# Kernel tuning notes

Measured on AMD Instinct MI355X. Metric: run time of the kernel, lower is better.

The kernel has to match this reference:

```python
import jax, jax.numpy as jnp
import numpy as np

N = 50000      # nodes
E = 400000     # edges (before self loops)
IN = 128       # in_channels
H = 4          # num_heads (layers 1-2)
C = 32         # hidden_dim per head
HID = H * C    # 128 total hidden
CLS = 40       # num_classes (out_heads = 1)
EPS = 1e-5     # BatchNorm eps
SLOPE = 0.2    # LeakyReLU negative slope (PyG GATConv default)


def setup_inputs() -> dict:
    key = jax.random.key(0)
    ks = jax.random.split(key, 24)
    rn = lambda k, shp, s: jax.random.normal(k, shp, jnp.float32) * s
    x = jax.random.normal(ks[0], (N, IN), jnp.float32)
    src = jax.random.randint(ks[1], (E,), 0, N)
    dst = jax.random.randint(ks[2], (E,), 0, N)
    src = jnp.where(src == dst, (src + 1) % N, src)  # no pre-existing self loops
    edge_index = jnp.stack([src, dst]).astype(jnp.int32)
    inp = dict(x=x, edge_index=edge_index)
    # conv1: in IN -> H heads x C
    inp['W1'] = rn(ks[3], (IN, H * C), 1.0 / np.sqrt(IN))
    inp['as1'] = rn(ks[4], (H, C), 0.1)
    inp['ad1'] = rn(ks[5], (H, C), 0.1)
    inp['b1'] = rn(ks[6], (H * C,), 0.02)
    # conv2: HID -> H x C
    inp['W2'] = rn(ks[7], (HID, H * C), 1.0 / np.sqrt(HID))
    inp['as2'] = rn(ks[8], (H, C), 0.1)
    inp['ad2'] = rn(ks[9], (H, C), 0.1)
    inp['b2'] = rn(ks[10], (H * C,), 0.02)
    # conv3: HID -> 1 head x CLS, concat=False
    inp['W3'] = rn(ks[11], (HID, CLS), 1.0 / np.sqrt(HID))
    inp['as3'] = rn(ks[12], (1, CLS), 0.1)
    inp['ad3'] = rn(ks[13], (1, CLS), 0.1)
    inp['b3'] = rn(ks[14], (CLS,), 0.02)
    # residual projection
    inp['Wres'] = rn(ks[15], (IN, HID), 1.0 / np.sqrt(IN))
    # BatchNorm (eval mode: running stats)
    inp['g1'] = 1.0 + rn(ks[16], (HID,), 0.1)
    inp['be1'] = rn(ks[17], (HID,), 0.1)
    inp['m1'] = rn(ks[18], (HID,), 0.1)
    inp['v1'] = 1.0 + jax.random.uniform(ks[19], (HID,), jnp.float32) * 0.5
    inp['g2'] = 1.0 + rn(ks[20], (HID,), 0.1)
    inp['be2'] = rn(ks[21], (HID,), 0.1)
    inp['m2'] = rn(ks[22], (HID,), 0.1)
    inp['v2'] = 1.0 + jax.random.uniform(ks[23], (HID,), jnp.float32) * 0.5
    return inp


def _gat_conv(h, src, dst, W, a_src, a_dst, bias, heads, out_ch, concat):
    """PyG-style GATConv (eval: attention dropout off), self loops already in src/dst."""
    n = h.shape[0]
    xw = (h @ W).reshape(n, heads, out_ch)                    # [N,H,C]
    e_src = jnp.sum(xw * a_src, axis=-1)                      # [N,H]
    e_dst = jnp.sum(xw * a_dst, axis=-1)                      # [N,H]
    e = jax.nn.leaky_relu(e_src[src] + e_dst[dst], SLOPE)     # [E',H]
    # segment softmax over incoming edges of each dst node
    mseg = jax.ops.segment_max(e, dst, num_segments=n)        # [N,H]
    ex = jnp.exp(e - mseg[dst])
    den = jax.ops.segment_sum(ex, dst, num_segments=n)
    alpha = ex / den[dst]                                     # [E',H]
    out = jax.ops.segment_sum(alpha[:, :, None] * xw[src], dst, num_segments=n)  # [N,H,C]
    out = out.reshape(n, heads * out_ch) if concat else out.mean(axis=1)
    return out + bias


def _bn(h, g, b, m, v):
    return (h - m) * jax.lax.rsqrt(v + EPS) * g + b


def reference(x, edge_index, W1, as1, ad1, b1, W2, as2, ad2, b2,
              W3, as3, ad3, b3, Wres, g1, be1, m1, v1, g2, be2, m2, v2):
    n = x.shape[0]
    loop = jnp.arange(n, dtype=edge_index.dtype)
    src = jnp.concatenate([edge_index[0], loop])  # add self loops (PyG default)
    dst = jnp.concatenate([edge_index[1], loop])
    x0 = x
    h = _gat_conv(x0, src, dst, W1, as1, ad1, b1, H, C, True)
    h = jax.nn.elu(_bn(h, g1, be1, m1, v1) + x0 @ Wres)
    h_res = h
    h = _gat_conv(h, src, dst, W2, as2, ad2, b2, H, C, True)
    h = jax.nn.elu(_bn(h, g2, be2, m2, v2) + h_res)
    logits = _gat_conv(h, src, dst, W3, as3, ad3, b3, 1, CLS, False)
    return logits
```

## Files before the change

### kernel.cpp

```cpp
#include <hip/hip_runtime.h>
#include <hip/hip_bf16.h>

#define THREADS 256

typedef __attribute__((ext_vector_type(8))) short bfrag;
typedef __attribute__((ext_vector_type(4))) float f32x4;

__device__ inline unsigned short f2b(float v) {
    __hip_bfloat16 b = __float2bfloat16(v);
    return *reinterpret_cast<unsigned short*>(&b);
}
__device__ inline float b2f(unsigned short u) {
    return __uint_as_float(((unsigned)u) << 16);
}
__device__ inline float rdv(const void* p, int off, bool isbf) {
    return isbf ? b2f(((const unsigned short*)p)[off]) : ((const float*)p)[off];
}
__device__ inline float dot8(const void* W, const void* av, int wbase, int abase, bool isbf) {
    if (isbf) {
        const unsigned short* wp = (const unsigned short*)W + wbase;
        const unsigned short* ap = (const unsigned short*)av + abase;
        ushort4 w0 = *(const ushort4*)wp, w1 = *(const ushort4*)(wp + 4);
        ushort4 a0 = *(const ushort4*)ap, a1 = *(const ushort4*)(ap + 4);
        return b2f(w0.x) * b2f(a0.x) + b2f(w0.y) * b2f(a0.y) +
               b2f(w0.z) * b2f(a0.z) + b2f(w0.w) * b2f(a0.w) +
               b2f(w1.x) * b2f(a1.x) + b2f(w1.y) * b2f(a1.y) +
               b2f(w1.z) * b2f(a1.z) + b2f(w1.w) * b2f(a1.w);
    } else {
        const float* wp = (const float*)W + wbase;
        const float* ap = (const float*)av + abase;
        float4 w0 = *(const float4*)wp, w1 = *(const float4*)(wp + 4);
        float4 a0 = *(const float4*)ap, a1 = *(const float4*)(ap + 4);
        return w0.x * a0.x + w0.y * a0.y + w0.z * a0.z + w0.w * a0.w +
               w1.x * a1.x + w1.y * a1.y + w1.z * a1.z + w1.w * a1.w;
    }
}

struct InPtrs { const void* p[23]; };

__global__ void prep_kernel(InPtrs in, int* __restrict__ flag,
                            unsigned short* __restrict__ Wl1, unsigned short* __restrict__ Wl2,
                            unsigned short* __restrict__ WlR, unsigned short* __restrict__ Wl3,
                            float* __restrict__ bnsc1, float* __restrict__ bnsh1,
                            float* __restrict__ bnsc2, float* __restrict__ bnsh2,
                            float* __restrict__ B3f,
                            int N, const int* __restrict__ ei, int* __restrict__ deg8,
                            int E, int DB) {
    int b = blockIdx.x, tid = threadIdx.x;
    if (b >= 30) {
        int stride = DB * 256;
        for (int i = (b - 30) * 256 + tid; i < E + N; i += stride) {
            int d = (i < E) ? ei[E + i] : (i - E);
            int k = (i >> 10) & 7;
            atomicAdd(&deg8[k * N + d], 1);
        }
        return;
    }
    __shared__ int sred[4];
    __shared__ float sWes[128 * 8];
    const unsigned short* x = (const unsigned short*)in.p[0];
    int local = 0;
    for (int i = tid; i < 4096; i += 256) {
        unsigned ex = (x[i] >> 7) & 0xFF;
        if (ex == 0xFF || ex >= 134 || (ex > 0 && ex <= 100)) local++;
    }
#pragma unroll
    for (int o = 1; o < 64; o <<= 1) local += __shfl_xor(local, o, 64);
    if ((tid & 63) == 0) sred[tid >> 6] = local;
    __syncthreads();
    bool isbf = !((sred[0] + sred[1] + sred[2] + sred[3]) * 8 > 4096);

    if (b < 29) {
        const void *Wv, *asp = 0, *adp = 0; unsigned short* o; int cols, FH = 0, tt;
        if (b < 9)       { Wv = in.p[2];  asp = in.p[3];  adp = in.p[4];  o = Wl1; cols = 128; FH = 4; tt = b; }
        else if (b < 18) { Wv = in.p[6];  asp = in.p[7];  adp = in.p[8];  o = Wl2; cols = 128; FH = 4; tt = b - 9; }
        else if (b < 26) { Wv = in.p[14];                                 o = WlR; cols = 128;         tt = b - 18; }
        else             { Wv = in.p[10]; asp = in.p[11]; adp = in.p[12]; o = Wl3; cols = 40;  FH = 1; tt = b - 26; }
        bool foldblk = (FH == 4 && tt == 8) || (FH == 1 && tt == 2);
        if (foldblk) {
            if (FH == 4) {
#pragma unroll
                for (int u = 0; u < 4; ++u) {
                    int od = tid * 4 + u;
                    int k = od >> 3, dn = od & 7;
                    int h = dn < 4 ? dn : dn - 4;
                    const void* av = dn < 4 ? asp : adp;
                    float s = 0.f;
#pragma unroll
                    for (int cc = 0; cc < 32; cc += 8)
                        s += dot8(Wv, av, k * 128 + h * 32 + cc, h * 32 + cc, isbf);
                    sWes[k * 8 + dn] = s;
                }
            } else {
                int k = tid >> 1, dn = tid & 1;
                const void* av = dn ? adp : asp;
                float s = 0.f;
#pragma unroll
                for (int cc = 0; cc < 40; cc += 8)
                    s += dot8(Wv, av, k * 40 + cc, cc, isbf);
                sWes[k * 8 + dn] = s;
            }
            __syncthreads();
        }
        int id = tt * 256 + tid;
        int ks = (id >> 6) & 3, l = id & 63;
        int q = l >> 4, n = l & 15;
        int c = tt * 16 + n;
#pragma unroll
        for (int j = 0; j < 8; ++j) {
            int k = ks * 32 + q * 8 + j;
            float v = 0.f;
            if (c < cols) v = rdv(Wv, k * cols + c, isbf);
            else if (FH && c < cols + 2 * FH) v = sWes[k * 8 + (c - cols)];
            o[id * 8 + j] = f2b(v);
        }
    } else {
        int c = tid;
        if (c < 128) {
            float s = rdv(in.p[15], c, isbf) * rsqrtf(rdv(in.p[18], c, isbf) + 1e-5f);
            bnsc1[c] = s;
            bnsh1[c] = rdv(in.p[16], c, isbf) - rdv(in.p[17], c, isbf) * s +
                       rdv(in.p[5], c, isbf) * s;
        } else {
            int d = c - 128;
            float s = rdv(in.p[19], d, isbf) * rsqrtf(rdv(in.p[22], d, isbf) + 1e-5f);
            bnsc2[d] = s;
            bnsh2[d] = rdv(in.p[20], d, isbf) - rdv(in.p[21], d, isbf) * s +
                       rdv(in.p[9], d, isbf) * s;
            if (d < 40) B3f[d] = rdv(in.p[13], d, isbf);
        }
        if (tid == 0) *flag = isbf ? 1 : 0;
    }
}

__global__ void bsum_kernel(const int* __restrict__ deg8, int* __restrict__ bsum, int N) {
    int idx = blockIdx.x * 256 + threadIdx.x;
    int lane = threadIdx.x & 63, wv = threadIdx.x >> 6;
    int v = 0;
    if (idx < N) {
#pragma unroll
        for (int k = 0; k < 8; ++k) v += deg8[k * N + idx];
    }
#pragma unroll
    for (int o = 1; o < 64; o <<= 1) v += __shfl_xor(v, o, 64);
    __shared__ int ws[4];
    if (lane == 0) ws[wv] = v;
    __syncthreads();
    if (threadIdx.x == 0) bsum[blockIdx.x] = ws[0] + ws[1] + ws[2] + ws[3];
}

__global__ __launch_bounds__(1024) void bscan_kernel(const int* __restrict__ bsum,
                                                     int* __restrict__ boff, int nb) {
    __shared__ int ws[16];
    int tid = threadIdx.x, lane = tid & 63, wv = tid >> 6;
    int v = (tid < nb) ? bsum[tid] : 0;
    int sc = v;
#pragma unroll
    for (int o = 1; o < 64; o <<= 1) {
        int t = __shfl_up(sc, o, 64);
        if (lane >= o) sc += t;
    }
    if (lane == 63) ws[wv] = sc;
    __syncthreads();
    int add = 0;
#pragma unroll
    for (int k = 0; k < 16; ++k) add += (k < wv) ? ws[k] : 0;
    if (tid < nb) boff[tid] = add + sc - v;
}

__global__ void scanw_kernel(const int* __restrict__ deg8, const int* __restrict__ boff,
                             int* __restrict__ row_ptr, int* __restrict__ posk, int N) {
    int idx = blockIdx.x * 256 + threadIdx.x;
    int lane = threadIdx.x & 63, wv = threadIdx.x >> 6;
    int vk[8];
    int v = 0;
    if (idx < N) {
#pragma unroll
        for (int k = 0; k < 8; ++k) { vk[k] = deg8[k * N + idx]; v += vk[k]; }
    } else {
#pragma unroll
        for (int k = 0; k < 8; ++k) vk[k] = 0;
    }
    int sc = v;
#pragma unroll
    for (int o = 1; o < 64; o <<= 1) {
        int t = __shfl_up(sc, o, 64);
        if (lane >= o) sc += t;
    }
    __shared__ int ws[4];
    if (lane == 63) ws[wv] = sc;
    __syncthreads();
    int add = boff[blockIdx.x];
#pragma unroll
    for (int k = 0; k < 4; ++k) add += (k < wv) ? ws[k] : 0;
    int excl = add + sc - v;
    if (idx < N) {
        row_ptr[idx + 1] = excl + v;
        int run = excl;
#pragma unroll
        for (int k = 0; k < 8; ++k) { posk[k * N + idx] = run; run += vk[k]; }
    }
    if (idx == 0) row_ptr[0] = 0;
}

__global__ __launch_bounds__(256) void fused_sg(
    const void* __restrict__ Ain, const int* __restrict__ flag,
    const unsigned short* __restrict__ Wg1, const unsigned short* __restrict__ WgR,
    unsigned short* __restrict__ xwb, unsigned short* __restrict__ resb,
    float* __restrict__ es, float* __restrict__ ed,
    const int* __restrict__ ei, int* __restrict__ posk, int* __restrict__ csr,
    int E, int N, int GG, int DB) {
    int tid = threadIdx.x;
    if ((int)blockIdx.x >= GG) {
        int sb = blockIdx.x - GG;
        int stride = DB * 256;
        for (int i = sb * 256 + tid; i < E + N; i += stride) {
            int s, d;
            if (i < E) { s = ei[i]; d = ei[E + i]; }
            else { s = i - E; d = s; }
            int k = (i >> 10) & 7;
            int p = atomicAdd(&posk[k * N + d], 1);
            csr[p] = s;
        }
        return;
    }
    __shared__ __align__(16) unsigned short Wls[16 * 2048];
    {
        const float4* s1 = (const float4*)Wg1;
        const float4* s2 = (const float4*)WgR;
        float4* dst = (float4*)Wls;
#pragma unroll
        for (int i = 0; i < 8; ++i) dst[tid + i * 256] = s1[tid + i * 256];
#pragma unroll
        for (int i = 0; i < 8; ++i) dst[2048 + tid + i * 256] = s2[tid + i * 256];
    }
    bool isbf = (*flag != 0);
    __syncthreads();
    int w = tid >> 6, lane = tid & 63;
    int n = lane & 15, q = lane >> 4;
    int row0 = blockIdx.x * 64 + w * 16;
    int ar = row0 + n; ar = ar < N ? ar : N - 1;
    bfrag a[4];
    if (isbf) {
        const unsigned short* arow = (const unsigned short*)Ain + (size_t)ar * 128;
#pragma unroll
        for (int ks = 0; ks < 4; ++ks)
            a[ks] = *reinterpret_cast<const bfrag*>(arow + ks * 32 + q * 8);
    } else {
        const float* arow = (const float*)Ain + (size_t)ar * 128;
#pragma unroll
        for (int ks = 0; ks < 4; ++ks) {
            float4 f0 = *reinterpret_cast<const float4*>(arow + ks * 32 + q * 8);
            float4 f1 = *reinterpret_cast<const float4*>(arow + ks * 32 + q * 8 + 4);
            bfrag t;
            t[0] = (short)f2b(f0.x); t[1] = (short)f2b(f0.y);
            t[2] = (short)f2b(f0.z); t[3] = (short)f2b(f0.w);
            t[4] = (short)f2b(f1.x); t[5] = (short)f2b(f1.y);
            t[6] = (short)f2b(f1.z); t[7] = (short)f2b(f1.w);
            a[ks] = t;
        }
    }
    f32x4 acc[16], accE;
#pragma unroll
    for (int t = 0; t < 16; ++t) acc[t] = (f32x4){0.f, 0.f, 0.f, 0.f};
    accE = (f32x4){0.f, 0.f, 0.f, 0.f};
#pragma unroll
    for (int ks = 0; ks < 4; ++ks) {
#pragma unroll
        for (int t = 0; t < 8; ++t) {
            bfrag b = *reinterpret_cast<const bfrag*>(&Wls[((t * 4 + ks) * 64 + lane) * 8]);
            acc[t] = __builtin_amdgcn_mfma_f32_16x16x32_bf16(a[ks], b, acc[t], 0, 0, 0);
        }
        bfrag be = *reinterpret_cast<const bfrag*>(Wg1 + ((size_t)(32 + ks) * 64 + lane) * 8);
        accE = __builtin_amdgcn_mfma_f32_16x16x32_bf16(a[ks], be, accE, 0, 0, 0);
#pragma unroll
        for (int t = 0; t < 8; ++t) {
            bfrag b = *reinterpret_cast<const bfrag*>(&Wls[16384 + ((t * 4 + ks) * 64 + lane) * 8]);
            acc[8 + t] = __builtin_amdgcn_mfma_f32_16x16x32_bf16(a[ks], b, acc[8 + t], 0, 0, 0);
        }
    }
#pragma unroll
    for (int r = 0; r < 4; ++r) {
        int row = row0 + q * 4 + r;
        if (row < N) {
            if (n < 4) es[(size_t)row * 4 + n] = accE[r];
            else if (n < 8) ed[(size_t)row * 4 + (n - 4)] = accE[r];
        }
    }
#pragma unroll
    for (int t = 0; t < 8; ++t) {
        int col = t * 16 + n;
#pragma unroll
        for (int r = 0; r < 4; ++r) {
            int row = row0 + q * 4 + r;
            if (row < N) {
                xwb[(size_t)row * 128 + col] = f2b(acc[t][r]);
                resb[(size_t)row * 128 + col] = f2b(acc[8 + t][r]);
            }
        }
    }
}

template <int COLT, int HEADS, int ESCOL>
__global__ __launch_bounds__(256) void gemm_mfma(
    const unsigned short* __restrict__ A, const unsigned short* __restrict__ Wg,
    unsigned short* __restrict__ out, int ldc, int cols,
    float* __restrict__ es, float* __restrict__ ed, int N) {
    __shared__ __align__(16) unsigned short Wls[COLT * 2048];
    int tid = threadIdx.x;
    {
        const float4* src = (const float4*)Wg;
        float4* dst = (float4*)Wls;
#pragma unroll
        for (int i = 0; i < COLT; ++i) dst[tid + i * 256] = src[tid + i * 256];
    }
    __syncthreads();
    int w = tid >> 6, lane = tid & 63;
    int n = lane & 15, q = lane >> 4;
    int row0 = blockIdx.x * 64 + w * 16;
    int ar = row0 + n; ar = ar < N ? ar : N - 1;
    f32x4 acc[COLT];
#pragma unroll
    for (int t = 0; t < COLT; ++t) acc[t] = (f32x4){0.f, 0.f, 0.f, 0.f};
    const unsigned short* arow = A + (size_t)ar * 128;
#pragma unroll
    for (int ks = 0; ks < 4; ++ks) {
        bfrag a = *reinterpret_cast<const bfrag*>(arow + ks * 32 + q * 8);
#pragma unroll
        for (int t = 0; t < COLT; ++t) {
            bfrag b = *reinterpret_cast<const bfrag*>(&Wls[((t * 4 + ks) * 64 + lane) * 8]);
            acc[t] = __builtin_amdgcn_mfma_f32_16x16x32_bf16(a, b, acc[t], 0, 0, 0);
        }
    }
    constexpr int TE = ESCOL >> 4, NE = ESCOL & 15;
    int dn = n - NE;
#pragma unroll
    for (int r = 0; r < 4; ++r) {
        int row = row0 + q * 4 + r;
        if (row < N) {
            if (dn >= 0 && dn < HEADS) es[(size_t)row * HEADS + dn] = acc[TE][r];
            else if (dn >= HEADS && dn < 2 * HEADS)
                ed[(size_t)row * HEADS + (dn - HEADS)] = acc[TE][r];
        }
    }
#pragma unroll
    for (int t = 0; t < COLT; ++t) {
        int col = t * 16 + n;
        if (col < cols) {
#pragma unroll
            for (int r = 0; r < 4; ++r) {
                int row = row0 + q * 4 + r;
                if (row < N) out[(size_t)row * ldc + col] = f2b(acc[t][r]);
            }
        }
    }
}

__global__ __launch_bounds__(256) void agg128_fused(
    const unsigned short* __restrict__ xwb, const float* __restrict__ es,
    const float* __restrict__ ed, const int* __restrict__ row_ptr,
    const int* __restrict__ csr, const float* __restrict__ bnsc,
    const float* __restrict__ bnsh, const unsigned short* __restrict__ resb,
    unsigned short* __restrict__ outb, int N) {
    int w = threadIdx.x >> 6, lane = threadIdx.x & 63;
    int node = blockIdx.x * 4 + w;
    if (node >= N) return;
    int h = lane >> 4;
    int c0 = lane * 2;
    float edl = ed[node * 4 + h];
    int start = __builtin_amdgcn_readfirstlane(row_ptr[node]);
    int end = __builtin_amdgcn_readfirstlane(row_ptr[node + 1]);
    float den = 0.f, a0 = 0.f, a1 = 0.f;
    for (int jb = start; jb < end; jb += 16) {
        int su[16];
#pragma unroll
        for (int u = 0; u < 16; ++u) {
            int idx = jb + u;
            idx = idx < end - 1 ? idx : end - 1;
            su[u] = csr[idx];
        }
        unsigned uu[16];
        float ev[16];
#pragma unroll
        for (int u = 0; u < 16; ++u) {
            uu[u] = *(const unsigned*)(xwb + (size_t)su[u] * 128 + c0);
            ev[u] = es[su[u] * 4 + h];
        }
#pragma unroll
        for (int u = 0; u < 16; ++u) {
            float e = ev[u] + edl;
            e = e > 0.f ? e : 0.2f * e;
            float wg = __expf(e);
            wg = (jb + u < end) ? wg : 0.f;
            den += wg;
            a0 = fmaf(wg, __uint_as_float(uu[u] << 16), a0);
            a1 = fmaf(wg, __uint_as_float(uu[u] & 0xffff0000u), a1);
        }
    }
    float inv = 1.f / den;
    float2 sc = *(const float2*)(bnsc + c0);
    float2 sh = *(const float2*)(bnsh + c0);
    unsigned ur = *(const unsigned*)(resb + (size_t)node * 128 + c0);
    float v0 = fmaf(a0 * inv, sc.x, sh.x) + __uint_as_float(ur << 16);
    float v1 = fmaf(a1 * inv, sc.y, sh.y) + __uint_as_float(ur & 0xffff0000u);
    v0 = v0 > 0.f ? v0 : expm1f(v0);
    v1 = v1 > 0.f ? v1 : expm1f(v1);
    unsigned pk = (unsigned)f2b(v0) | ((unsigned)f2b(v1) << 16);
    *(unsigned*)(outb + (size_t)node * 128 + c0) = pk;
}

__global__ __launch_bounds__(256) void agg40_kernel(
    const unsigned short* __restrict__ xw3b, const float* __restrict__ es3,
    const float* __restrict__ ed3, const int* __restrict__ row_ptr,
    const int* __restrict__ csr, const float* __restrict__ b3,
    void* __restrict__ out, const int* __restrict__ flag, int N) {
    int w = threadIdx.x >> 6, lane = threadIdx.x & 63;
    int node = blockIdx.x * 4 + w;
    if (node >= N) return;
    int i16 = lane & 15;
    int g = lane >= 40 ? 2 : (lane >= 20 ? 1 : 0);
    int cp = lane - g * 20;
    int c0 = cp * 2; c0 = c0 > 38 ? 38 : c0;
    float edl = ed3[node];
    int start = row_ptr[node], end = row_ptr[node + 1];
    float den = 0.f, a0 = 0.f, a1 = 0.f;
    for (int jb = start; jb < end; jb += 16) {
        int cnt = end - jb; cnt = cnt < 16 ? cnt : 16;
        int sv = csr[jb + (i16 < cnt ? i16 : 0)];
        unsigned uu[6];
#pragma unroll
        for (int t = 0; t < 6; ++t) {
            int slot = 3 * t + g; slot = slot < 15 ? slot : 15;
            int s = __shfl(sv, slot, 64);
            uu[t] = *(const unsigned*)(xw3b + (size_t)s * 40 + c0);
        }
        float wgl = 0.f;
        if (i16 < cnt) {
            float e = es3[sv] + edl;
            e = e > 0.f ? e : 0.2f * e;
            wgl = __expf(e);
        }
        float d = wgl;
        d += __shfl_xor(d, 1, 64);
        d += __shfl_xor(d, 2, 64);
        d += __shfl_xor(d, 4, 64);
        d += __shfl_xor(d, 8, 64);
        den += d;
#pragma unroll
        for (int t = 0; t < 6; ++t) {
            int slot = 3 * t + g;
            int sl = slot < 15 ? slot : 15;
            float wg = __shfl(wgl, sl, 64);
            if (slot >= cnt) wg = 0.f;
            a0 = fmaf(wg, __uint_as_float(uu[t] << 16), a0);
            a1 = fmaf(wg, __uint_as_float(uu[t] & 0xffff0000u), a1);
        }
    }
    float t0 = __shfl(a0, (lane + 20) & 63, 64);
    float t1 = __shfl(a0, (lane + 40) & 63, 64);
    float u0 = __shfl(a1, (lane + 20) & 63, 64);
    float u1 = __shfl(a1, (lane + 40) & 63, 64);
    a0 += t0 + t1;
    a1 += u0 + u1;
    if (lane < 20) {
        float inv = 1.f / den;
        float v0 = a0 * inv + b3[c0];
        float v1 = a1 * inv + b3[c0 + 1];
        size_t eoff = (size_t)node * 40 + c0;
        if (*flag) {
            unsigned pk = (unsigned)f2b(v0) | ((unsigned)f2b(v1) << 16);
            *(unsigned*)((unsigned short*)out + eoff) = pk;
        } else {
            *(float2*)((float*)out + eoff) = make_float2(v0, v1);
        }
    }
}

extern "C" void kernel_launch(void* const* d_in, const int* in_sizes, int n_in,
                              void* d_out, int out_size, void* d_ws, size_t ws_size,
                              hipStream_t stream) {
    (void)n_in; (void)out_size; (void)ws_size;
    const int N = in_sizes[0] / 128;
    const int E = in_sizes[1] / 2;
    const int EPN = E + N;
    const int NB = (N + 255) / 256;
    const int DB = (EPN + 511) / 512;
    char* base = (char*)d_ws;
    size_t off = 0;
    auto alloc = [&](size_t bytes) -> char* {
        char* p = base + off;
        off = (off + bytes + 255) & ~(size_t)255;
        return p;
    };
    int* flag = (int*)alloc(4);
    int* deg8 = (int*)alloc((size_t)N * 8 * 4);
    int* posk = (int*)alloc((size_t)N * 8 * 4);
    int* row_ptr = (int*)alloc((size_t)(N + 1) * 4);
    int* bsum = (int*)alloc((size_t)NB * 4);
    int* boff = (int*)alloc((size_t)NB * 4);
    int* csr = (int*)alloc((size_t)EPN * 4);
    float* bnsc1 = (float*)alloc(512); float* bnsh1 = (float*)alloc(512);
    float* bnsc2 = (float*)alloc(512); float* bnsh2 = (float*)alloc(512);
    float* B3f = (float*)alloc(256);
    unsigned short* Wl1 = (unsigned short*)alloc(36864);
    unsigned short* Wl2 = (unsigned short*)alloc(36864);
    unsigned short* WlR = (unsigned short*)alloc(32768);
    unsigned short* Wl3 = (unsigned short*)alloc(12288);
    unsigned short* xwb = (unsigned short*)alloc((size_t)N * 128 * 2);
    unsigned short* h1b = (unsigned short*)alloc((size_t)N * 128 * 2);
    unsigned short* resb = (unsigned short*)alloc((size_t)N * 128 * 2);
    float* es = (float*)alloc((size_t)N * 4 * 4);
    float* ed = (float*)alloc((size_t)N * 4 * 4);

    const int* ei = (const int*)d_in[1];

    hipMemsetAsync(deg8, 0, (size_t)N * 8 * 4, stream);

    InPtrs ip;
    for (int t = 0; t < 23; t++) ip.p[t] = d_in[t];
    prep_kernel<<<30 + DB, THREADS, 0, stream>>>(ip, flag, Wl1, Wl2, WlR, Wl3,
                                                 bnsc1, bnsh1, bnsc2, bnsh2,
                                                 B3f, N, ei, deg8, E, DB);

    bsum_kernel<<<NB, 256, 0, stream>>>(deg8, bsum, N);
    bscan_kernel<<<1, 1024, 0, stream>>>(bsum, boff, NB);
    scanw_kernel<<<NB, 256, 0, stream>>>(deg8, boff, row_ptr, posk, N);

    int gemmGrid = (N + 63) / 64;
    int aggGrid = (N + 3) / 4;

    fused_sg<<<gemmGrid + DB, 256, 0, stream>>>(d_in[0], flag, Wl1, WlR,
                                                xwb, resb, es, ed,
                                                ei, posk, csr, E, N, gemmGrid, DB);
    agg128_fused<<<aggGrid, 256, 0, stream>>>(xwb, es, ed, row_ptr, csr,
                                              bnsc1, bnsh1, resb, h1b, N);
    gemm_mfma<9, 4, 128><<<gemmGrid, 256, 0, stream>>>(
        h1b, Wl2, xwb, 128, 128, es, ed, N);
    unsigned short* h2b = resb;
    agg128_fused<<<aggGrid, 256, 0, stream>>>(xwb, es, ed, row_ptr, csr,
                                              bnsc2, bnsh2, h1b, h2b, N);
    gemm_mfma<3, 1, 40><<<gemmGrid, 256, 0, stream>>>(
        h2b, Wl3, xwb, 40, 40, es, ed, N);
    agg40_kernel<<<aggGrid, 256, 0, stream>>>(xwb, es, ed, row_ptr, csr, B3f,
                                              d_out, flag, N);
}
```

Measured before the change: 275.9 us.

## Split agg128 wavefront into four edge groups with 16-byte feature loads

The 128-wide aggregation kernel now gives each quarter of the wavefront its own subset of edges, and each lane loads 8 bf16 channels at once with 16-byte loads instead of 2. Partial sums are combined with xor shuffles at the end, and only the first group applies the epilogue and writes. This spreads the per-edge exp and gather work across lanes so fewer serial iterations are needed per node, at the cost of 8 accumulators per lane and a cross-lane reduction. The batchnorm, residual and bias loads are also hoisted ahead of the edge loop in both aggregation kernels so they overlap the gathers.

```diff
diff --git a/kernel.cpp b/kernel.cpp
--- a/kernel.cpp
+++ b/kernel.cpp
@@ -365,48 +365,68 @@
     int w = threadIdx.x >> 6, lane = threadIdx.x & 63;
     int node = blockIdx.x * 4 + w;
     if (node >= N) return;
-    int h = lane >> 4;
-    int c0 = lane * 2;
+    int eg = lane >> 4;
+    int cp = lane & 15;
+    int c0 = cp * 8;
+    int h = cp >> 2;
     float edl = ed[node * 4 + h];
+    float4 scA = *(const float4*)(bnsc + c0);
+    float4 scB = *(const float4*)(bnsc + c0 + 4);
+    float4 shA = *(const float4*)(bnsh + c0);
+    float4 shB = *(const float4*)(bnsh + c0 + 4);
+    bfrag ur = *(const bfrag*)(resb + (size_t)node * 128 + c0);
     int start = __builtin_amdgcn_readfirstlane(row_ptr[node]);
     int end = __builtin_amdgcn_readfirstlane(row_ptr[node + 1]);
-    float den = 0.f, a0 = 0.f, a1 = 0.f;
+    float den = 0.f;
+    float acc[8];
+#pragma unroll
+    for (int i = 0; i < 8; ++i) acc[i] = 0.f;
     for (int jb = start; jb < end; jb += 16) {
-        int su[16];
-#pragma unroll
-        for (int u = 0; u < 16; ++u) {
-            int idx = jb + u;
+        int su[4];
+#pragma unroll
+        for (int u4 = 0; u4 < 4; ++u4) {
+            int idx = jb + u4 * 4 + eg;
             idx = idx < end - 1 ? idx : end - 1;
-            su[u] = csr[idx];
-        }
-        unsigned uu[16];
-        float ev[16];
-#pragma unroll
-        for (int u = 0; u < 16; ++u) {
-            uu[u] = *(const unsigned*)(xwb + (size_t)su[u] * 128 + c0);
-            ev[u] = es[su[u] * 4 + h];
-        }
-#pragma unroll
-        for (int u = 0; u < 16; ++u) {
-            float e = ev[u] + edl;
+            su[u4] = csr[idx];
+        }
+        bfrag uu[4];
+        float ev[4];
+#pragma unroll
+        for (int u4 = 0; u4 < 4; ++u4) {
+            uu[u4] = *(const bfrag*)(xwb + (size_t)su[u4] * 128 + c0);
+            ev[u4] = es[su[u4] * 4 + h];
+        }
+#pragma unroll
+        for (int u4 = 0; u4 < 4; ++u4) {
+            float e = ev[u4] + edl;
             e = e > 0.f ? e : 0.2f * e;
             float wg = __expf(e);
-            wg = (jb + u < end) ? wg : 0.f;
+            wg = (jb + u4 * 4 + eg < end) ? wg : 0.f;
             den += wg;
-            a0 = fmaf(wg, __uint_as_float(uu[u] << 16), a0);
-            a1 = fmaf(wg, __uint_as_float(uu[u] & 0xffff0000u), a1);
-        }
-    }
-    float inv = 1.f / den;
-    float2 sc = *(const float2*)(bnsc + c0);
-    float2 sh = *(const float2*)(bnsh + c0);
-    unsigned ur = *(const unsigned*)(resb + (size_t)node * 128 + c0);
-    float v0 = fmaf(a0 * inv, sc.x, sh.x) + __uint_as_float(ur << 16);
-    float v1 = fmaf(a1 * inv, sc.y, sh.y) + __uint_as_float(ur & 0xffff0000u);
-    v0 = v0 > 0.f ? v0 : expm1f(v0);
-    v1 = v1 > 0.f ? v1 : expm1f(v1);
-    unsigned pk = (unsigned)f2b(v0) | ((unsigned)f2b(v1) << 16);
-    *(unsigned*)(outb + (size_t)node * 128 + c0) = pk;
+#pragma unroll
+            for (int i = 0; i < 8; ++i)
+                acc[i] = fmaf(wg, b2f((unsigned short)uu[u4][i]), acc[i]);
+        }
+    }
+#pragma unroll
+    for (int o = 16; o <= 32; o <<= 1) {
+        den += __shfl_xor(den, o, 64);
+#pragma unroll
+        for (int i = 0; i < 8; ++i) acc[i] += __shfl_xor(acc[i], o, 64);
+    }
+    if (eg == 0) {
+        float inv = 1.f / den;
+        float scv[8] = {scA.x, scA.y, scA.z, scA.w, scB.x, scB.y, scB.z, scB.w};
+        float shv[8] = {shA.x, shA.y, shA.z, shA.w, shB.x, shB.y, shB.z, shB.w};
+        bfrag pk;
+#pragma unroll
+        for (int i = 0; i < 8; ++i) {
+            float v = fmaf(acc[i] * inv, scv[i], shv[i]) + b2f((unsigned short)ur[i]);
+            v = v > 0.f ? v : expm1f(v);
+            pk[i] = (short)f2b(v);
+        }
+        *(bfrag*)(outb + (size_t)node * 128 + c0) = pk;
+    }
 }
 
 __global__ __launch_bounds__(256) void agg40_kernel(
@@ -422,6 +442,7 @@
     int cp = lane - g * 20;
     int c0 = cp * 2; c0 = c0 > 38 ? 38 : c0;
     float edl = ed3[node];
+    float b30 = b3[c0], b31 = b3[c0 + 1];
     int start = row_ptr[node], end = row_ptr[node + 1];
     float den = 0.f, a0 = 0.f, a1 = 0.f;
     for (int jb = start; jb < end; jb += 16) {
@@ -464,8 +485,8 @@
     a1 += u0 + u1;
     if (lane < 20) {
         float inv = 1.f / den;
-        float v0 = a0 * inv + b3[c0];
-        float v1 = a1 * inv + b3[c0 + 1];
+        float v0 = a0 * inv + b30;
+        float v1 = a1 * inv + b31;
         size_t eoff = (size_t)node * 40 + c0;
         if (*flag) {
             unsigned pk = (unsigned)f2b(v0) | ((unsigned)f2b(v1) << 16);
```

Measured after the change: 280.2 us. No clear change (+1.5%).
